# Kernel optimization log

Measured on AMD Instinct MI355X. Metric: run time of the kernel, lower is better.

The kernel has to match this reference:

```python
import math
import jax, jax.numpy as jnp
import numpy as np

B, T, C = 2, 2048, 1024
H, HKV, HD = 16, 4, 64  # n_head, n_kv_head, head_dim
G = H // HKV            # GQA groups
WS = 1024               # sliding window size
GATE_CH = 32


def setup_inputs() -> dict:
    key = jax.random.key(0)
    ks = jax.random.split(key, 8)
    x = jax.random.normal(ks[0], (B, T, C), dtype=jnp.float32)
    ve = jax.random.normal(ks[1], (B, T, HKV * HD), dtype=jnp.float32)
    # realistic RoPE tables: half head_dim frequencies
    d = HD // 2
    inv_freq = 1.0 / (10000.0 ** (jnp.arange(d, dtype=jnp.float32) / d))
    angles = jnp.arange(T, dtype=jnp.float32)[:, None] * inv_freq[None, :]  # (T, d)
    cos = jnp.cos(angles)[None, :, None, :]  # (1, T, 1, d)
    sin = jnp.sin(angles)[None, :, None, :]
    s = 0.02
    Wq = s * jax.random.normal(ks[2], (C, H * HD), dtype=jnp.float32)
    Wk = s * jax.random.normal(ks[3], (C, HKV * HD), dtype=jnp.float32)
    Wv = s * jax.random.normal(ks[4], (C, HKV * HD), dtype=jnp.float32)
    Wproj = s * jax.random.normal(ks[5], (C, C), dtype=jnp.float32)
    Wg = s * jax.random.normal(ks[6], (GATE_CH, HKV), dtype=jnp.float32)
    return {"x": x, "ve": ve, "cos": cos, "sin": sin,
            "Wq": Wq, "Wk": Wk, "Wv": Wv, "Wproj": Wproj, "Wg": Wg, "ws": WS}


def _rope(u, cos, sin):
    d = u.shape[-1] // 2
    u1, u2 = u[..., :d], u[..., d:]
    return jnp.concatenate([u1 * cos + u2 * sin, -u1 * sin + u2 * cos], axis=-1)


def _rmsnorm(u):
    eps = jnp.finfo(u.dtype).eps
    return u * jax.lax.rsqrt(jnp.mean(u * u, axis=-1, keepdims=True) + eps)


def reference(x, ve, cos, sin, Wq, Wk, Wv, Wproj, Wg, ws):
    b, t, c = x.shape
    q = (x @ Wq).reshape(b, t, H, HD)
    k = (x @ Wk).reshape(b, t, HKV, HD)
    v = (x @ Wv).reshape(b, t, HKV, HD)
    # value-embedding gate: 2*sigmoid over first 32 channels of x
    gate = 2.0 * jax.nn.sigmoid(x[..., :GATE_CH] @ Wg)  # (b, t, HKV)
    v = v + gate[..., None] * ve.reshape(b, t, HKV, HD)
    q = _rmsnorm(_rope(q, cos, sin))
    k = _rmsnorm(_rope(k, cos, sin))
    # GQA: view q as (b, t, HKV, G, HD), contract against shared k/v per kv-head
    qg = q.reshape(b, t, HKV, G, HD)
    scale = 1.0 / math.sqrt(HD)
    scores = jnp.einsum('bqhgd,bkhd->bhgqk', qg, k) * scale  # (b, HKV, G, t, t)
    pos = jnp.arange(t)
    # key j attends iff i - ws + 1 <= j <= i (sliding causal window)
    mask = (pos[None, :] >= pos[:, None] - ws + 1) & (pos[None, :] <= pos[:, None])
    scores = jnp.where(mask[None, None, None], scores, -jnp.inf)
    attn = jax.nn.softmax(scores, axis=-1)
    y = jnp.einsum('bhgqk,bkhd->bqhgd', attn, v).reshape(b, t, H * HD)
    return y @ Wproj
```

## Files before the change

### kernel.cpp

```cpp
#include <hip/hip_runtime.h>
#include <hip/hip_bf16.h>

#define Bq 2
#define Tq 2048
#define Cq 1024
#define Hq 16
#define HKVq 4
#define HDq 64
#define Gq 4
#define WSq 1024
#define GATE_CHq 32

typedef __attribute__((ext_vector_type(8))) short short8;
typedef __attribute__((ext_vector_type(4))) float f32x4;
typedef __attribute__((ext_vector_type(2))) unsigned int u32x2;
typedef unsigned int u32;
typedef unsigned short u16;

#if __has_builtin(__builtin_amdgcn_exp2f)
#define EXP2(x) __builtin_amdgcn_exp2f(x)
#else
#define EXP2(x) exp2f(x)
#endif

__device__ __forceinline__ u16 f2bf(float f) {
  u32 u = __float_as_uint(f);
  u32 r = (u + 0x7FFFu + ((u >> 16) & 1u)) >> 16;
  return (u16)r;
}
__device__ __forceinline__ float bf2f(u16 u) {
  return __uint_as_float(((u32)u) << 16);
}

__device__ __forceinline__ void gl_lds16(const u16* g, u16* l) {
  __builtin_amdgcn_global_load_lds(
      (const u32 __attribute__((address_space(1)))*)g,
      (u32 __attribute__((address_space(3)))*)l, 16, 0, 0);
}

template <bool BF16OUT>
__global__ __launch_bounds__(256) void gemm_bt(
    const u16* __restrict__ A, const u16* __restrict__ Bt,
    void* __restrict__ Cv, int M, int N, int K) {
  __shared__ __attribute__((aligned(16))) u16 As[64 * 64];
  __shared__ __attribute__((aligned(16))) u16 Bs[128 * 64];

  const int bm0 = blockIdx.y * 64, bn0 = blockIdx.x * 128;
  const int tid = threadIdx.x;
  const int w = tid >> 6, lane = tid & 63;
  const int wm = (w >> 1) * 32, wn = (w & 1) * 64;
  const int quad = lane >> 4, l16 = lane & 15;

  f32x4 acc[2][4];
#pragma unroll
  for (int mt = 0; mt < 2; mt++)
#pragma unroll
    for (int nt = 0; nt < 4; nt++) acc[mt][nt] = (f32x4){0.f, 0.f, 0.f, 0.f};

  int goffA[2], goffB[4];
#pragma unroll
  for (int i = 0; i < 2; i++) {
    int s = i * 256 + tid;
    int m = s >> 3, gp = s & 7;
    goffA[i] = m * K + (gp ^ (m & 7)) * 8;
  }
#pragma unroll
  for (int i = 0; i < 4; i++) {
    int s = i * 256 + tid;
    int m = s >> 3, gp = s & 7;
    goffB[i] = m * K + (gp ^ (m & 7)) * 8;
  }
  const u16* Ab = A + (long)bm0 * K;
  const u16* Bb = Bt + (long)bn0 * K;

  for (int k0 = 0; k0 < K; k0 += 64) {
    __syncthreads();
#pragma unroll
    for (int i = 0; i < 2; i++)
      gl_lds16(Ab + goffA[i] + k0, &As[(i * 256 + w * 64) * 8]);
#pragma unroll
    for (int i = 0; i < 4; i++)
      gl_lds16(Bb + goffB[i] + k0, &Bs[(i * 256 + w * 64) * 8]);
    __syncthreads();

#pragma unroll
    for (int ks = 0; ks < 2; ks++) {
      short8 af[2], bf[4];
#pragma unroll
      for (int mt = 0; mt < 2; mt++) {
        int ml = wm + mt * 16 + l16;
        af[mt] = *(const short8*)&As[ml * 64 + (((ks * 4 + quad) ^ (ml & 7)) * 8)];
      }
#pragma unroll
      for (int nt = 0; nt < 4; nt++) {
        int nl = wn + nt * 16 + l16;
        bf[nt] = *(const short8*)&Bs[nl * 64 + (((ks * 4 + quad) ^ (nl & 7)) * 8)];
      }
#pragma unroll
      for (int mt = 0; mt < 2; mt++)
#pragma unroll
        for (int nt = 0; nt < 4; nt++)
          acc[mt][nt] = __builtin_amdgcn_mfma_f32_16x16x32_bf16(
              af[mt], bf[nt], acc[mt][nt], 0, 0, 0);
    }
  }

#pragma unroll
  for (int mt = 0; mt < 2; mt++)
#pragma unroll
    for (int nt = 0; nt < 4; nt++) {
      int row0 = bm0 + wm + mt * 16 + quad * 4;
      int col = bn0 + wn + nt * 16 + l16;
#pragma unroll
      for (int r = 0; r < 4; r++) {
        if (BF16OUT)
          ((u16*)Cv)[(long)(row0 + r) * N + col] = f2bf(acc[mt][nt][r]);
        else
          ((float*)Cv)[(long)(row0 + r) * N + col] = acc[mt][nt][r];
      }
    }
}

__global__ __launch_bounds__(256) void prep(
    const float* __restrict__ x, u16* __restrict__ xb,
    const float* __restrict__ Wq, const float* __restrict__ Wk,
    const float* __restrict__ Wv, const float* __restrict__ Wproj,
    u16* __restrict__ Dqkv, u16* __restrict__ Dproj) {
  __shared__ float tile[64][65];
  int bx = blockIdx.x;
  int tid = threadIdx.x;
  if (bx < 2048) {
    int i = (bx * 256 + tid) * 8;
    float4 a = *(const float4*)(x + i);
    float4 b = *(const float4*)(x + i + 4);
    union { short8 v; u16 u[8]; } o;
    o.u[0] = f2bf(a.x); o.u[1] = f2bf(a.y); o.u[2] = f2bf(a.z); o.u[3] = f2bf(a.w);
    o.u[4] = f2bf(b.x); o.u[5] = f2bf(b.y); o.u[6] = f2bf(b.z); o.u[7] = f2bf(b.w);
    *(short8*)(xb + i) = o.v;
    return;
  }
  int wb = bx - 2048;
  int obx = wb >> 4;
  int k0 = (wb & 15) * 64;
  const float* S;
  u16* Dst;
  int N, nb;
  if (obx < 16)      { S = Wq;    N = 1024; nb = obx;      Dst = Dqkv; }
  else if (obx < 20) { S = Wk;    N = 256;  nb = obx - 16; Dst = Dqkv + 1024 * 1024; }
  else if (obx < 24) { S = Wv;    N = 256;  nb = obx - 20; Dst = Dqkv + 1280 * 1024; }
  else               { S = Wproj; N = 1024; nb = obx - 24; Dst = Dproj; }
  int n0 = nb * 64;
#pragma unroll
  for (int i = 0; i < 16; i++) {
    int idx = i * 256 + tid;
    int kl = idx >> 6, nl = idx & 63;
    tile[kl][nl] = S[(long)(k0 + kl) * N + n0 + nl];
  }
  __syncthreads();
#pragma unroll
  for (int i = 0; i < 16; i++) {
    int idx = i * 256 + tid;
    int nl = idx >> 6, kl = idx & 63;
    Dst[(long)(n0 + nl) * 1024 + k0 + kl] = f2bf(tile[kl][nl]);
  }
}

__device__ __forceinline__ float rope_rms(float u, int lane, float c, float s) {
  float up = __shfl_xor(u, 32);
  float r = (lane < 32) ? (u * c + up * s) : (u * c - up * s);
  float sum = r * r;
#pragma unroll
  for (int off = 32; off >= 1; off >>= 1) sum += __shfl_xor(sum, off);
  return r * rsqrtf(sum * (1.f / 64.f) + 1.1920928955078125e-07f);
}

__global__ __launch_bounds__(256) void postproc2(
    const float* __restrict__ x, const float* __restrict__ ve,
    const float* __restrict__ cosp, const float* __restrict__ sinp,
    const float* __restrict__ Wg, const u16* __restrict__ QKV,
    u16* __restrict__ Qb, u16* __restrict__ Kb, u16* __restrict__ Vtb) {
  __shared__ u16 vt[64][70];
  int bh = blockIdx.y;
  int b = bh >> 2, hkv = bh & 3;
  int t0 = blockIdx.x * 64;
  int tid = threadIdx.x;
  int w = tid >> 6, lane = tid & 63;

  for (int tt = 0; tt < 16; tt++) {
    int tl = tt * 4 + w;
    int t = t0 + tl;
    long bt = (long)b * Tq + t;
    const u16* row = QKV + bt * 1536;
    float c = cosp[t * 32 + (lane & 31)];
    float s = sinp[t * 32 + (lane & 31)];

    float pg = 0.f;
    if (lane < 32) pg = x[bt * Cq + lane] * Wg[lane * HKVq + hkv];
#pragma unroll
    for (int off = 16; off >= 1; off >>= 1) pg += __shfl_xor(pg, off);
    float gate = 2.f / (1.f + expf(-__shfl(pg, 0)));

    float v = bf2f(row[1280 + hkv * 64 + lane]) +
              gate * ve[bt * 256 + hkv * 64 + lane];
    vt[tl][lane] = f2bf(v);

    float kv = rope_rms(bf2f(row[1024 + hkv * 64 + lane]), lane, c, s);
    Kb[((long)bh * Tq + t) * 64 + lane] = f2bf(kv);

#pragma unroll
    for (int g = 0; g < 4; g++) {
      float q = rope_rms(bf2f(row[(hkv * 4 + g) * 64 + lane]), lane, c, s);
      Qb[((long)(bh * 4 + g) * Tq + t) * 64 + lane] = f2bf(q);
    }
  }
  __syncthreads();
#pragma unroll
  for (int i = 0; i < 16; i++) {
    int idx = i * 256 + tid;
    int d = idx >> 6, tl = idx & 63;
    Vtb[(long)bh * 64 * Tq + (long)d * Tq + t0 + tl] = vt[tl][d];
  }
}

#define CEXP 0.18033688011112042f
#define CEXP8 1.4426950408889634f

template <bool MASK>
__device__ __forceinline__ void attn_half(
    int k0h, int key_base, int vg_base, int q0, int quad, int l16,
    const u16* __restrict__ Ks, const u16* __restrict__ Vts,
    u32* __restrict__ myPs, const short8 (&QB)[2][2], f32x4 (&O)[2][4],
    float (&lsum)[2]) {
  f32x4 S4[4][2];
#pragma unroll
  for (int kt4 = 0; kt4 < 4; kt4++) {
    int key = key_base + kt4 * 16 + l16;
    short8 kb0 = *(const short8*)(&Ks[key * 64 + ((quad ^ (key & 7)) * 8)]);
    short8 kb1 = *(const short8*)(&Ks[key * 64 + (((4 + quad) ^ (key & 7)) * 8)]);
#pragma unroll
    for (int qj = 0; qj < 2; qj++) {
      f32x4 acc = (f32x4){0.f, 0.f, 0.f, 0.f};
      acc = __builtin_amdgcn_mfma_f32_16x16x32_bf16(kb0, QB[qj][0], acc, 0, 0, 0);
      acc = __builtin_amdgcn_mfma_f32_16x16x32_bf16(kb1, QB[qj][1], acc, 0, 0, 0);
      S4[kt4][qj] = acc;
    }
  }

#pragma unroll
  for (int kt4 = 0; kt4 < 4; kt4++)
#pragma unroll
    for (int qj = 0; qj < 2; qj++) {
      float Pv[4];
#pragma unroll
      for (int r = 0; r < 4; r++) {
        float sv = S4[kt4][qj][r];
        if (MASK) {
          int kpos = k0h + kt4 * 16 + quad * 4 + r;
          int qpos = q0 + qj * 16 + l16;
          bool valid = (kpos <= qpos) && (kpos >= qpos - (WSq - 1));
          sv = valid ? sv : -1e30f;
        }
        float p = EXP2(__builtin_fmaf(sv, CEXP, -CEXP8));
        Pv[r] = p;
        lsum[qj] += p;
      }
      u32x2 pk;
#pragma unroll
      for (int rp = 0; rp < 2; rp++) {
        u32 lo = __float_as_uint(Pv[2 * rp]) + 0x8000u;
        u32 hi = __float_as_uint(Pv[2 * rp + 1]) + 0x8000u;
        pk[rp] = __builtin_amdgcn_perm(hi, lo, 0x07060302u);
      }
      *(u32x2*)(&myPs[(qj * 16 + l16) * 36 + kt4 * 8 + quad * 2]) = pk;
    }

  short8 vb[4][2];
#pragma unroll
  for (int nt = 0; nt < 4; nt++) {
    int d = nt * 16 + l16;
    vb[nt][0] = *(const short8*)(&Vts[d * 128 + (((vg_base + quad) ^ (d & 7)) * 8)]);
    vb[nt][1] =
        *(const short8*)(&Vts[d * 128 + (((vg_base + 4 + quad) ^ (d & 7)) * 8)]);
  }

#pragma unroll
  for (int qj = 0; qj < 2; qj++) {
    const u32* prow = &myPs[(qj * 16 + l16) * 36];
    short8 pa0 = *(const short8*)(prow + quad * 4);
    short8 pa1 = *(const short8*)(prow + 16 + quad * 4);
#pragma unroll
    for (int nt = 0; nt < 4; nt++) {
      O[qj][nt] =
          __builtin_amdgcn_mfma_f32_16x16x32_bf16(pa0, vb[nt][0], O[qj][nt], 0, 0, 0);
      O[qj][nt] =
          __builtin_amdgcn_mfma_f32_16x16x32_bf16(pa1, vb[nt][1], O[qj][nt], 0, 0, 0);
    }
  }
}

__global__ __launch_bounds__(256, 2) void attn_mfma(
    const u16* __restrict__ Qb, const u16* __restrict__ Kb,
    const u16* __restrict__ Vtb, u16* __restrict__ Yb) {
  __shared__ __attribute__((aligned(16))) u16 Ks[128 * 64];
  __shared__ __attribute__((aligned(16))) u16 Vts[64 * 128];
  __shared__ __attribute__((aligned(16))) u32 Ps[4][2][32 * 36];

  int bid = blockIdx.x;
  int bh = bid & 7;
  int qt32 = bid >> 3;
  int hkv = bh & 3;
  int b = bh >> 2;
  int q0 = qt32 * 32;
  int tid = threadIdx.x;
  int g = tid >> 6;
  int lane = tid & 63;
  int quad = lane >> 4;
  int l16 = lane & 15;

  short8 QB[2][2];
#pragma unroll
  for (int qj = 0; qj < 2; qj++) {
    const u16* qb =
        Qb + ((long)((bh * 4 + g) * Tq + q0 + qj * 16 + l16)) * 64 + quad * 8;
    QB[qj][0] = *(const short8*)(qb);
    QB[qj][1] = *(const short8*)(qb + 32);
  }

  f32x4 O[2][4];
#pragma unroll
  for (int qj = 0; qj < 2; qj++)
#pragma unroll
    for (int nt = 0; nt < 4; nt++) O[qj][nt] = (f32x4){0.f, 0.f, 0.f, 0.f};
  float lsum[2] = {0.f, 0.f};

  int lo = q0 - (WSq - 1);
  int st = (lo < 0 ? 0 : lo) >> 7;
  int et = (q0 + 31) >> 7;

  const u16* Kbase = Kb + ((long)bh * Tq) * 64;
  const u16* Vbase = Vtb + ((long)bh * 64) * Tq;

  int rowoffK[4], rowoffV[4];
#pragma unroll
  for (int i = 0; i < 4; i++) {
    int s = i * 256 + tid;
    int kr = s >> 3, kgp = s & 7;
    rowoffK[i] = kr * 64 + (kgp ^ (kr & 7)) * 8;
    int d = s >> 4, vgp = s & 15;
    rowoffV[i] = d * Tq + (vgp ^ (d & 7)) * 8;
  }

  for (int kt = st; kt <= et; kt++) {
    int k0 = kt << 7;
    __syncthreads();
#pragma unroll
    for (int i = 0; i < 4; i++) {
      gl_lds16(Kbase + (long)k0 * 64 + rowoffK[i], &Ks[(i * 256 + g * 64) * 8]);
      gl_lds16(Vbase + k0 + rowoffV[i], &Vts[(i * 256 + g * 64) * 8]);
    }
    __syncthreads();

    bool needC = (k0 + 127 > q0);
    bool needW = (k0 < q0 - 992);
    if (needC || needW) {
      attn_half<true>(k0, 0, 0, q0, quad, l16, Ks, Vts, &Ps[g][0][0], QB, O, lsum);
      attn_half<true>(k0 + 64, 64, 8, q0, quad, l16, Ks, Vts, &Ps[g][1][0], QB,
                      O, lsum);
    } else {
      attn_half<false>(k0, 0, 0, q0, quad, l16, Ks, Vts, &Ps[g][0][0], QB, O,
                       lsum);
      attn_half<false>(k0 + 64, 64, 8, q0, quad, l16, Ks, Vts, &Ps[g][1][0], QB,
                       O, lsum);
    }
  }

#pragma unroll
  for (int qj = 0; qj < 2; qj++) {
    lsum[qj] += __shfl_xor(lsum[qj], 16);
    lsum[qj] += __shfl_xor(lsum[qj], 32);
  }

  int h = hkv * 4 + g;
#pragma unroll
  for (int qj = 0; qj < 2; qj++) {
    float invl[4];
#pragma unroll
    for (int r = 0; r < 4; r++) invl[r] = 1.f / __shfl(lsum[qj], quad * 4 + r);
#pragma unroll
    for (int nt = 0; nt < 4; nt++)
#pragma unroll
      for (int r = 0; r < 4; r++)
        Yb[((long)(b * Tq + q0 + qj * 16 + quad * 4 + r)) * 1024 + h * 64 +
           nt * 16 + l16] = f2bf(O[qj][nt][r] * invl[r]);
  }
}

extern "C" void kernel_launch(void* const* d_in, const int* in_sizes, int n_in,
                              void* d_out, int out_size, void* d_ws,
                              size_t ws_size, hipStream_t stream) {
  const float* x     = (const float*)d_in[0];
  const float* ve    = (const float*)d_in[1];
  const float* cosp  = (const float*)d_in[2];
  const float* sinp  = (const float*)d_in[3];
  const float* Wq    = (const float*)d_in[4];
  const float* Wk    = (const float*)d_in[5];
  const float* Wv    = (const float*)d_in[6];
  const float* Wproj = (const float*)d_in[7];
  const float* Wg    = (const float*)d_in[8];

  char* base = (char*)d_ws;
  u16* xb     = (u16*)(base);
  u16* Qb     = xb;
  u16* WqkvT  = (u16*)(base + 8388608);
  u16* Kb     = WqkvT;
  u16* WprojT = (u16*)(base + 11534336);
  u16* QKVb   = (u16*)(base + 13631488);
  u16* Vtb    = (u16*)(base + 26214400);
  u16* Yb     = (u16*)(base + 28311552);
  float* out = (float*)d_out;

  prep<<<2688, 256, 0, stream>>>(x, xb, Wq, Wk, Wv, Wproj, WqkvT, WprojT);
  gemm_bt<true><<<dim3(12, 64), 256, 0, stream>>>(xb, WqkvT, QKVb, 4096, 1536,
                                                  1024);
  postproc2<<<dim3(32, 8), 256, 0, stream>>>(x, ve, cosp, sinp, Wg, QKVb, Qb,
                                             Kb, Vtb);
  attn_mfma<<<512, 256, 0, stream>>>(Qb, Kb, Vtb, Yb);
  gemm_bt<false><<<dim3(8, 64), 256, 0, stream>>>(Yb, WprojT, out, 4096, 1024,
                                                  1024);
}
```

Measured before the change: 183.2 us.

## Fuse RoPE, RMSNorm, value gate and V transpose into QKV GEMM epilogue

The QKV GEMM epilogue now applies RoPE and RMSNorm to Q/K tiles in registers, using shuffles across the 16-lane groups that hold one head row. For V tiles it adds the gated value embedding and writes V already transposed. The gate sigmoid moves into extra blocks of the prep kernel, written to a small buffer. This removes the postproc kernel launch and the round trip of the bf16 QKV intermediate through global memory. In exchange the epilogue stores are narrower and more scattered, and the workspace layout is reorganised.

```diff
diff --git a/kernel.cpp b/kernel.cpp
--- a/kernel.cpp
+++ b/kernel.cpp
@@ -38,10 +38,149 @@
       (u32 __attribute__((address_space(3)))*)l, 16, 0, 0);
 }
 
-template <bool BF16OUT>
-__global__ __launch_bounds__(256) void gemm_bt(
+__global__ __launch_bounds__(256) void qkv_gemm_fused(
     const u16* __restrict__ A, const u16* __restrict__ Bt,
-    void* __restrict__ Cv, int M, int N, int K) {
+    const float* __restrict__ ve, const float* __restrict__ cosp,
+    const float* __restrict__ sinp, const float* __restrict__ gatebuf,
+    u16* __restrict__ Qb, u16* __restrict__ Kb, u16* __restrict__ Vtb) {
+  __shared__ __attribute__((aligned(16))) u16 As[64 * 64];
+  __shared__ __attribute__((aligned(16))) u16 Bs[128 * 64];
+
+  const int bx = blockIdx.x;
+  const int bm0 = blockIdx.y * 64, bn0 = bx * 128;
+  const int tid = threadIdx.x;
+  const int w = tid >> 6, lane = tid & 63;
+  const int wm = (w >> 1) * 32, wn = (w & 1) * 64;
+  const int quad = lane >> 4, l16 = lane & 15;
+  const int K = 1024;
+
+  f32x4 acc[2][4];
+#pragma unroll
+  for (int mt = 0; mt < 2; mt++)
+#pragma unroll
+    for (int nt = 0; nt < 4; nt++) acc[mt][nt] = (f32x4){0.f, 0.f, 0.f, 0.f};
+
+  int goffA[2], goffB[4];
+#pragma unroll
+  for (int i = 0; i < 2; i++) {
+    int s = i * 256 + tid;
+    int m = s >> 3, gp = s & 7;
+    goffA[i] = m * K + (gp ^ (m & 7)) * 8;
+  }
+#pragma unroll
+  for (int i = 0; i < 4; i++) {
+    int s = i * 256 + tid;
+    int m = s >> 3, gp = s & 7;
+    goffB[i] = m * K + (gp ^ (m & 7)) * 8;
+  }
+  const u16* Ab = A + (long)bm0 * K;
+  const u16* Bb = Bt + (long)bn0 * K;
+
+  for (int k0 = 0; k0 < K; k0 += 64) {
+    __syncthreads();
+#pragma unroll
+    for (int i = 0; i < 2; i++)
+      gl_lds16(Ab + goffA[i] + k0, &As[(i * 256 + w * 64) * 8]);
+#pragma unroll
+    for (int i = 0; i < 4; i++)
+      gl_lds16(Bb + goffB[i] + k0, &Bs[(i * 256 + w * 64) * 8]);
+    __syncthreads();
+
+#pragma unroll
+    for (int ks = 0; ks < 2; ks++) {
+      short8 af[2], bf[4];
+#pragma unroll
+      for (int mt = 0; mt < 2; mt++) {
+        int ml = wm + mt * 16 + l16;
+        af[mt] = *(const short8*)&As[ml * 64 + (((ks * 4 + quad) ^ (ml & 7)) * 8)];
+      }
+#pragma unroll
+      for (int nt = 0; nt < 4; nt++) {
+        int nl = wn + nt * 16 + l16;
+        bf[nt] = *(const short8*)&Bs[nl * 64 + (((ks * 4 + quad) ^ (nl & 7)) * 8)];
+      }
+#pragma unroll
+      for (int mt = 0; mt < 2; mt++)
+#pragma unroll
+        for (int nt = 0; nt < 4; nt++)
+          acc[mt][nt] = __builtin_amdgcn_mfma_f32_16x16x32_bf16(
+              af[mt], bf[nt], acc[mt][nt], 0, 0, 0);
+    }
+  }
+
+  const int b = bm0 >> 11;
+  const int tseq0 = (bm0 & 2047) + wm;
+
+  if (bx < 10) {
+    u16* Dst;
+    if (bx < 8) {
+      int hh = bx * 2 + (w & 1);
+      int hkv = hh >> 2, g = hh & 3;
+      Dst = Qb + ((long)((b * 4 + hkv) * 4 + g) * Tq) * 64;
+    } else {
+      int kk = (bx - 8) * 2 + (w & 1);
+      Dst = Kb + ((long)(b * 4 + kk) * Tq) * 64;
+    }
+#pragma unroll
+    for (int mt = 0; mt < 2; mt++) {
+#pragma unroll
+      for (int r = 0; r < 4; r++) {
+        int t = tseq0 + mt * 16 + quad * 4 + r;
+        float c0 = cosp[t * 32 + l16];
+        float s0 = sinp[t * 32 + l16];
+        float c1 = cosp[t * 32 + 16 + l16];
+        float s1 = sinp[t * 32 + 16 + l16];
+        float a0 = acc[mt][0][r], a1 = acc[mt][1][r];
+        float a2 = acc[mt][2][r], a3 = acc[mt][3][r];
+        float rp0 = a0 * c0 + a2 * s0;
+        float rp1 = a1 * c1 + a3 * s1;
+        float rp2 = a2 * c0 - a0 * s0;
+        float rp3 = a3 * c1 - a1 * s1;
+        float ss = rp0 * rp0 + rp1 * rp1 + rp2 * rp2 + rp3 * rp3;
+        ss += __shfl_xor(ss, 1);
+        ss += __shfl_xor(ss, 2);
+        ss += __shfl_xor(ss, 4);
+        ss += __shfl_xor(ss, 8);
+        float sc = rsqrtf(ss * (1.f / 64.f) + 1.1920928955078125e-07f);
+        u16* drow = Dst + (long)t * 64;
+        drow[l16] = f2bf(rp0 * sc);
+        drow[16 + l16] = f2bf(rp1 * sc);
+        drow[32 + l16] = f2bf(rp2 * sc);
+        drow[48 + l16] = f2bf(rp3 * sc);
+      }
+    }
+  } else {
+    int kk = (bx - 10) * 2 + (w & 1);
+    u16* Dst = Vtb + ((long)(b * 4 + kk) * 64) * Tq;
+#pragma unroll
+    for (int mt = 0; mt < 2; mt++) {
+      float vals[4][4];
+#pragma unroll
+      for (int r = 0; r < 4; r++) {
+        int t = tseq0 + mt * 16 + quad * 4 + r;
+        long bt = (long)b * Tq + t;
+        float gv = gatebuf[bt * 4 + kk];
+        const float* verow = ve + bt * 256 + kk * 64;
+#pragma unroll
+        for (int nt = 0; nt < 4; nt++)
+          vals[nt][r] = acc[mt][nt][r] + gv * verow[nt * 16 + l16];
+      }
+      int t0m = tseq0 + mt * 16 + quad * 4;
+#pragma unroll
+      for (int nt = 0; nt < 4; nt++) {
+        int d = nt * 16 + l16;
+        union { short4 v; u16 u[4]; } p;
+#pragma unroll
+        for (int r = 0; r < 4; r++) p.u[r] = f2bf(vals[nt][r]);
+        *(short4*)(Dst + (long)d * Tq + t0m) = p.v;
+      }
+    }
+  }
+}
+
+__global__ __launch_bounds__(256) void gemm_proj(
+    const u16* __restrict__ A, const u16* __restrict__ Bt,
+    float* __restrict__ C, int M, int N, int K) {
   __shared__ __attribute__((aligned(16))) u16 As[64 * 64];
   __shared__ __attribute__((aligned(16))) u16 Bs[128 * 64];
 
@@ -112,12 +251,8 @@
       int row0 = bm0 + wm + mt * 16 + quad * 4;
       int col = bn0 + wn + nt * 16 + l16;
 #pragma unroll
-      for (int r = 0; r < 4; r++) {
-        if (BF16OUT)
-          ((u16*)Cv)[(long)(row0 + r) * N + col] = f2bf(acc[mt][nt][r]);
-        else
-          ((float*)Cv)[(long)(row0 + r) * N + col] = acc[mt][nt][r];
-      }
+      for (int r = 0; r < 4; r++)
+        C[(long)(row0 + r) * N + col] = acc[mt][nt][r];
     }
 }
 
@@ -125,7 +260,8 @@
     const float* __restrict__ x, u16* __restrict__ xb,
     const float* __restrict__ Wq, const float* __restrict__ Wk,
     const float* __restrict__ Wv, const float* __restrict__ Wproj,
-    u16* __restrict__ Dqkv, u16* __restrict__ Dproj) {
+    const float* __restrict__ Wg, u16* __restrict__ Dqkv,
+    u16* __restrict__ Dproj, float* __restrict__ gatebuf) {
   __shared__ float tile[64][65];
   int bx = blockIdx.x;
   int tid = threadIdx.x;
@@ -139,6 +275,16 @@
     *(short8*)(xb + i) = o.v;
     return;
   }
+  if (bx >= 2688) {
+    int p = (bx - 2688) * 256 + tid;
+    int bt = p >> 2, kk = p & 3;
+    const float* xr = x + (long)bt * Cq;
+    float dot = 0.f;
+#pragma unroll
+    for (int i = 0; i < GATE_CHq; i++) dot += xr[i] * Wg[i * HKVq + kk];
+    gatebuf[p] = 2.f / (1.f + expf(-dot));
+    return;
+  }
   int wb = bx - 2048;
   int obx = wb >> 4;
   int k0 = (wb & 15) * 64;
@@ -162,63 +308,6 @@
     int idx = i * 256 + tid;
     int nl = idx >> 6, kl = idx & 63;
     Dst[(long)(n0 + nl) * 1024 + k0 + kl] = f2bf(tile[kl][nl]);
-  }
-}
-
-__device__ __forceinline__ float rope_rms(float u, int lane, float c, float s) {
-  float up = __shfl_xor(u, 32);
-  float r = (lane < 32) ? (u * c + up * s) : (u * c - up * s);
-  float sum = r * r;
-#pragma unroll
-  for (int off = 32; off >= 1; off >>= 1) sum += __shfl_xor(sum, off);
-  return r * rsqrtf(sum * (1.f / 64.f) + 1.1920928955078125e-07f);
-}
-
-__global__ __launch_bounds__(256) void postproc2(
-    const float* __restrict__ x, const float* __restrict__ ve,
-    const float* __restrict__ cosp, const float* __restrict__ sinp,
-    const float* __restrict__ Wg, const u16* __restrict__ QKV,
-    u16* __restrict__ Qb, u16* __restrict__ Kb, u16* __restrict__ Vtb) {
-  __shared__ u16 vt[64][70];
-  int bh = blockIdx.y;
-  int b = bh >> 2, hkv = bh & 3;
-  int t0 = blockIdx.x * 64;
-  int tid = threadIdx.x;
-  int w = tid >> 6, lane = tid & 63;
-
-  for (int tt = 0; tt < 16; tt++) {
-    int tl = tt * 4 + w;
-    int t = t0 + tl;
-    long bt = (long)b * Tq + t;
-    const u16* row = QKV + bt * 1536;
-    float c = cosp[t * 32 + (lane & 31)];
-    float s = sinp[t * 32 + (lane & 31)];
-
-    float pg = 0.f;
-    if (lane < 32) pg = x[bt * Cq + lane] * Wg[lane * HKVq + hkv];
-#pragma unroll
-    for (int off = 16; off >= 1; off >>= 1) pg += __shfl_xor(pg, off);
-    float gate = 2.f / (1.f + expf(-__shfl(pg, 0)));
-
-    float v = bf2f(row[1280 + hkv * 64 + lane]) +
-              gate * ve[bt * 256 + hkv * 64 + lane];
-    vt[tl][lane] = f2bf(v);
-
-    float kv = rope_rms(bf2f(row[1024 + hkv * 64 + lane]), lane, c, s);
-    Kb[((long)bh * Tq + t) * 64 + lane] = f2bf(kv);
-
-#pragma unroll
-    for (int g = 0; g < 4; g++) {
-      float q = rope_rms(bf2f(row[(hkv * 4 + g) * 64 + lane]), lane, c, s);
-      Qb[((long)(bh * 4 + g) * Tq + t) * 64 + lane] = f2bf(q);
-    }
-  }
-  __syncthreads();
-#pragma unroll
-  for (int i = 0; i < 16; i++) {
-    int idx = i * 256 + tid;
-    int d = idx >> 6, tl = idx & 63;
-    Vtb[(long)bh * 64 * Tq + (long)d * Tq + t0 + tl] = vt[tl][d];
   }
 }
 
@@ -409,22 +498,20 @@
   const float* Wg    = (const float*)d_in[8];
 
   char* base = (char*)d_ws;
-  u16* xb     = (u16*)(base);
-  u16* Qb     = xb;
-  u16* WqkvT  = (u16*)(base + 8388608);
-  u16* Kb     = WqkvT;
-  u16* WprojT = (u16*)(base + 11534336);
-  u16* QKVb   = (u16*)(base + 13631488);
-  u16* Vtb    = (u16*)(base + 26214400);
-  u16* Yb     = (u16*)(base + 28311552);
+  u16* xb      = (u16*)(base);
+  u16* Yb      = xb;
+  u16* WqkvT   = (u16*)(base + 8388608);
+  u16* WprojT  = (u16*)(base + 11534336);
+  u16* Qb      = (u16*)(base + 13631488);
+  u16* Kb      = (u16*)(base + 22020096);
+  u16* Vtb     = (u16*)(base + 24117248);
+  float* gateb = (float*)(base + 26214400);
   float* out = (float*)d_out;
 
-  prep<<<2688, 256, 0, stream>>>(x, xb, Wq, Wk, Wv, Wproj, WqkvT, WprojT);
-  gemm_bt<true><<<dim3(12, 64), 256, 0, stream>>>(xb, WqkvT, QKVb, 4096, 1536,
-                                                  1024);
-  postproc2<<<dim3(32, 8), 256, 0, stream>>>(x, ve, cosp, sinp, Wg, QKVb, Qb,
-                                             Kb, Vtb);
+  prep<<<2752, 256, 0, stream>>>(x, xb, Wq, Wk, Wv, Wproj, Wg, WqkvT, WprojT,
+                                 gateb);
+  qkv_gemm_fused<<<dim3(12, 64), 256, 0, stream>>>(xb, WqkvT, ve, cosp, sinp,
+                                                   gateb, Qb, Kb, Vtb);
   attn_mfma<<<512, 256, 0, stream>>>(Qb, Kb, Vtb, Yb);
-  gemm_bt<false><<<dim3(8, 64), 256, 0, stream>>>(Yb, WprojT, out, 4096, 1024,
-                                                  1024);
-}
+  gemm_proj<<<dim3(8, 64), 256, 0, stream>>>(Yb, WprojT, out, 4096, 1024, 1024);
+}
```

After: 162.2 us. 1.13x faster.
